# Optimization experiments

Measured on AMD Instinct MI355X. Metric: run time of the kernel, lower is better.

## Reference

```python
import jax, jax.numpy as jnp
import numpy as np
from jax import lax

D = 1024
T = 1024
B = 8


def setup_inputs() -> dict:
    key = jax.random.key(0)
    ks = jax.random.split(key, 4)
    x = jax.random.normal(ks[0], (T, B, D), dtype=jnp.float32)
    h0 = jnp.zeros((B, D), dtype=jnp.float32)
    # xavier-ish scale for input projections, small orthogonal-like scale for W_h
    xav = float(np.sqrt(2.0 / (D + D)))
    W_alpha = jax.random.normal(ks[1], (D, D), dtype=jnp.float32) * xav
    b_alpha = jnp.full((D,), 2.0, dtype=jnp.float32)  # init_alpha_bias=2.0
    W_h = jax.random.normal(ks[2], (D, D), dtype=jnp.float32) * (0.5 / np.sqrt(D))
    W_x = jax.random.normal(ks[3], (D, D), dtype=jnp.float32) * xav
    b = jnp.zeros((D,), dtype=jnp.float32)
    return {"x": x, "h0": h0, "W_alpha": W_alpha, "b_alpha": b_alpha,
            "W_h": W_h, "W_x": W_x, "b": b}


def reference(x, h0, W_alpha, b_alpha, W_h, W_x, b):
    # x: [T,B,D], h0: [B,D]; E63a nonlinear delta recurrence.
    # Precompute input-dependent parts (parallel over T), scan the recurrence.
    alpha_all = jax.nn.sigmoid(jnp.einsum('tbd,ed->tbe', x, W_alpha) + b_alpha)  # [T,B,D]
    wx_all = jnp.einsum('tbd,ed->tbe', x, W_x) + b                               # [T,B,D]

    def step(h_prev, inp):
        alpha, wx = inp
        v = jnp.tanh(h_prev @ W_h.T + wx)          # nonlinear value in h
        h_new = alpha * h_prev + (1.0 - alpha) * v  # complementary gate
        out = h_new * jax.nn.silu(h_new)            # gated output
        return h_new, (h_new, out)

    _, (hs, outs) = lax.scan(step, h0, (alpha_all, wx_all))
    h = jnp.concatenate([h0[None], hs], axis=0)  # [T+1,B,D] (matches torch path)
    return outs, h
```

## Files before the change

### kernel.cpp

```cpp
#include <hip/hip_runtime.h>
#include <hip/hip_bf16.h>
#include <hip/hip_cooperative_groups.h>

typedef __attribute__((ext_vector_type(8))) short bf16x8;
typedef __attribute__((ext_vector_type(4))) float f32x4;
typedef __attribute__((ext_vector_type(4))) unsigned int u32x4;

#define D_ 1024
#define T_ 1024
#define B_ 8
#define M_ (T_ * B_)

__device__ __forceinline__ float ldv(const float* p) { return *p; }
__device__ __forceinline__ float ldv(const __hip_bfloat16* p) { return __bfloat162float(*p); }
__device__ __forceinline__ void stv(float* p, float v) { *p = v; }
__device__ __forceinline__ void stv(__hip_bfloat16* p, float v) { *p = __float2bfloat16(v); }

__device__ __forceinline__ u32x4 ld_chunk(const unsigned* p) {
  u32x4 v;
  asm volatile("global_load_dwordx4 %0, %1, off sc0 sc1" : "=v"(v) : "v"(p) : "memory");
  return v;
}
__device__ __forceinline__ void st_word(unsigned* p, unsigned v) {
  asm volatile("global_store_dword %0, %1, off sc0 sc1" :: "v"(p), "v"(v) : "memory");
}
__device__ __forceinline__ void wait_vm0() {
  asm volatile("s_waitcnt vmcnt(0)" ::: "memory");
}
__device__ __forceinline__ void bar_lds() {
  asm volatile("s_waitcnt lgkmcnt(0)\n\ts_barrier" ::: "memory");
  __builtin_amdgcn_sched_barrier(0);
}

__global__ __launch_bounds__(256) void conv_bf16(const float* __restrict__ in,
                                                 __hip_bfloat16* __restrict__ out,
                                                 int n8)
{
  int i = blockIdx.x * blockDim.x + threadIdx.x;
  const int stride = gridDim.x * blockDim.x;
  for (; i < n8; i += stride) {
    const f32x4* p = reinterpret_cast<const f32x4*>(in + (size_t)i * 8);
    f32x4 a = p[0], b = p[1];
    union { bf16x8 v; __hip_bfloat16 e[8]; } u;
#pragma unroll
    for (int j = 0; j < 4; ++j) {
      u.e[j] = __float2bfloat16(a[j]);
      u.e[j + 4] = __float2bfloat16(b[j]);
    }
    *reinterpret_cast<bf16x8*>(out + (size_t)i * 8) = u.v;
  }
}

template <typename ST>
__global__ __launch_bounds__(256) void gemm_front(
    const __hip_bfloat16* __restrict__ xb,
    const __hip_bfloat16* __restrict__ Wab,
    const float* __restrict__ ba,
    const __hip_bfloat16* __restrict__ Wxb,
    const float* __restrict__ bbias,
    ST* __restrict__ alpha_out,
    ST* __restrict__ wx_out)
{
  const int tid = threadIdx.x;
  const int lane = tid & 63;
  const int w = tid >> 6;
  const int r = lane & 15;
  const int g = lane >> 4;
  const bool isA = blockIdx.y < 8;
  const int m0 = blockIdx.x * 128 + (w >> 1) * 64;
  const int n0 = (blockIdx.y & 7) * 128 + (w & 1) * 64;
  const __hip_bfloat16* __restrict__ W = isA ? Wab : Wxb;
  ST* __restrict__ outp = isA ? alpha_out : wx_out;

  f32x4 acc[4][4] = {};

  const __hip_bfloat16* aBase = xb + (size_t)(m0 + r) * D_ + g * 8;
  const __hip_bfloat16* bBase = W + (size_t)(n0 + r) * D_ + g * 8;

  for (int k = 0; k < D_; k += 32) {
    bf16x8 a[4], b[4];
#pragma unroll
    for (int mt = 0; mt < 4; ++mt)
      a[mt] = *reinterpret_cast<const bf16x8*>(aBase + (size_t)mt * 16 * D_ + k);
#pragma unroll
    for (int nt = 0; nt < 4; ++nt)
      b[nt] = *reinterpret_cast<const bf16x8*>(bBase + (size_t)nt * 16 * D_ + k);
#pragma unroll
    for (int mt = 0; mt < 4; ++mt)
#pragma unroll
      for (int nt = 0; nt < 4; ++nt)
        acc[mt][nt] = __builtin_amdgcn_mfma_f32_16x16x32_bf16(a[mt], b[nt], acc[mt][nt], 0, 0, 0);
  }

#pragma unroll
  for (int nt = 0; nt < 4; ++nt) {
    const int col = n0 + nt * 16 + r;
    const float bias = isA ? ba[col] : bbias[col];
#pragma unroll
    for (int mt = 0; mt < 4; ++mt) {
      const int row = m0 + mt * 16 + g * 4;
#pragma unroll
      for (int i = 0; i < 4; ++i) {
        float v = acc[mt][nt][i] + bias;
        if (isA) v = 1.0f / (1.0f + expf(-v));
        stv(outp + (size_t)(row + i) * D_ + col, v);
      }
    }
  }
}

template <typename ST>
__global__ __launch_bounds__(256) void scan_rec(
    const float* __restrict__ h0,
    const float* __restrict__ Wh,
    const ST* __restrict__ alpha_all,
    const ST* __restrict__ wx_all,
    unsigned* __restrict__ ring,
    float* __restrict__ out_outs,
    float* __restrict__ out_h)
{
  __shared__ __align__(16) unsigned short W_lds[64 * 1024];
  __shared__ __align__(16) unsigned short h_lds[1024];
  __shared__ float C_lds[4][64];

  const int tid = threadIdx.x;
  const int lane = tid & 63;
  const int w = tid >> 6;
  const int r = lane & 15;
  const int g = lane >> 4;
  const int bb = blockIdx.x & 7;
  const int s = blockIdx.x >> 3;
  const int e0 = s * 64;

  for (int idx = tid; idx < 64 * 128; idx += 256) {
    const int row = idx >> 7;
    const int k8 = (idx & 127) * 8;
    const f32x4* p = reinterpret_cast<const f32x4*>(Wh + (size_t)(e0 + row) * D_ + k8);
    f32x4 a = p[0], bv = p[1];
    union { bf16x8 v; __hip_bfloat16 e[8]; } u;
#pragma unroll
    for (int j = 0; j < 4; ++j) {
      u.e[j] = __float2bfloat16(a[j]);
      u.e[j + 4] = __float2bfloat16(bv[j]);
    }
    const unsigned byteoff = ((unsigned)row * 2048u + (unsigned)k8 * 2u) ^ (((unsigned)row & 7u) << 4);
    *reinterpret_cast<bf16x8*>(reinterpret_cast<char*>(W_lds) + byteoff) = u.v;
  }

  float h_f = 0.0f, wx_c = 0.0f, al_c = 0.0f;
  if (tid < 64) {
    const int e = e0 + tid;
    h_f = h0[bb * D_ + e];
    out_h[(size_t)bb * D_ + e] = h_f;
    const unsigned short hb = ((__hip_bfloat16_raw)__float2bfloat16(h_f)).x;
    h_lds[e] = hb;
    st_word(ring + (size_t)bb * 1024 + e, (unsigned)hb | (1u << 16));
    wx_c = ldv(wx_all + (size_t)bb * D_ + e);
    al_c = ldv(alpha_all + (size_t)bb * D_ + e);
  }
  __syncthreads();

  for (int t = 0; t < T_; ++t) {
    const unsigned want = (unsigned)(t + 1);
    const int kk = w * 256 + lane * 8;
    if (lane < 32 && (kk >> 6) != s) {
      const unsigned* cp = ring + ((size_t)(t & 1) * B_ + bb) * 1024 + kk;
      u32x4 A, Bv;
      int bail = 0;
      for (;;) {
        A = ld_chunk(cp);
        Bv = ld_chunk(cp + 4);
        wait_vm0();
        const bool ok = (A[0] >> 16) == want && (A[1] >> 16) == want &&
                        (A[2] >> 16) == want && (A[3] >> 16) == want &&
                        (Bv[0] >> 16) == want && (Bv[1] >> 16) == want &&
                        (Bv[2] >> 16) == want && (Bv[3] >> 16) == want;
        if (__all(ok)) break;
        if (++bail > (1 << 20)) break;
      }
      u32x4 hw;
      hw[0] = (A[0] & 0xffffu) | (A[1] << 16);
      hw[1] = (A[2] & 0xffffu) | (A[3] << 16);
      hw[2] = (Bv[0] & 0xffffu) | (Bv[1] << 16);
      hw[3] = (Bv[2] & 0xffffu) | (Bv[3] << 16);
      *reinterpret_cast<u32x4*>(&h_lds[kk]) = hw;
    }
    asm volatile("s_waitcnt lgkmcnt(0)" ::: "memory");
    __builtin_amdgcn_sched_barrier(0);

    f32x4 acc[4] = {};
#pragma unroll
    for (int kt = 0; kt < 8; ++kt) {
      const int k = w * 256 + kt * 32 + g * 8;
      bf16x8 afrag = {};
      if (r == 0)
        afrag = *reinterpret_cast<const bf16x8*>(&h_lds[k]);
#pragma unroll
      for (int nt = 0; nt < 4; ++nt) {
        const unsigned row = (unsigned)(nt * 16 + r);
        const unsigned byteoff = (row * 2048u + (unsigned)k * 2u) ^ ((row & 7u) << 4);
        bf16x8 bfrag = *reinterpret_cast<const bf16x8*>(
            reinterpret_cast<const char*>(W_lds) + byteoff);
        acc[nt] = __builtin_amdgcn_mfma_f32_16x16x32_bf16(afrag, bfrag, acc[nt], 0, 0, 0);
      }
    }
    if (g == 0) {
#pragma unroll
      for (int nt = 0; nt < 4; ++nt)
        C_lds[w][nt * 16 + r] = acc[nt][0];
    }
    bar_lds();

    if (tid < 64) {
      const int e = e0 + tid;
      const float y = C_lds[0][tid] + C_lds[1][tid] + C_lds[2][tid] + C_lds[3][tid];
      const float v = tanhf(y + wx_c);
      h_f = al_c * h_f + (1.0f - al_c) * v;
      const unsigned short hb = ((__hip_bfloat16_raw)__float2bfloat16(h_f)).x;
      h_lds[e] = hb;
      st_word(ring + ((size_t)((t + 1) & 1) * B_ + bb) * 1024 + e,
              (unsigned)hb | ((unsigned)(t + 2) << 16));
      const float sg = 1.0f / (1.0f + expf(-h_f));
      const float o = h_f * h_f * sg;
      out_h[(size_t)(t + 1) * (B_ * D_) + (size_t)bb * D_ + e] = h_f;
      out_outs[(size_t)t * (B_ * D_) + (size_t)bb * D_ + e] = o;
      if (t + 1 < T_) {
        wx_c = ldv(wx_all + (size_t)((t + 1) * B_ + bb) * D_ + e);
        al_c = ldv(alpha_all + (size_t)((t + 1) * B_ + bb) * D_ + e);
      }
    }
    bar_lds();
  }
}

template <typename ST>
static void launch_all(const float* x, const float* h0, const float* Wa,
                       const float* ba, const float* Wh, const float* Wx,
                       const float* bb, __hip_bfloat16* xb, __hip_bfloat16* Wab,
                       __hip_bfloat16* Wxb, ST* alpha_buf, ST* wx_buf,
                       unsigned* ring, float* out_outs, float* out_h,
                       hipStream_t stream)
{
  const size_t ringBytes = (size_t)2 * B_ * 1024 * 4;
  hipMemsetAsync(ring, 0, ringBytes, stream);
  conv_bf16<<<dim3(2048), dim3(256), 0, stream>>>(x, xb, M_ * D_ / 8);
  conv_bf16<<<dim3(512), dim3(256), 0, stream>>>(Wa, Wab, D_ * D_ / 8);
  conv_bf16<<<dim3(512), dim3(256), 0, stream>>>(Wx, Wxb, D_ * D_ / 8);
  gemm_front<ST><<<dim3(64, 16), dim3(256), 0, stream>>>(xb, Wab, ba, Wxb, bb,
                                                         alpha_buf, wx_buf);
  void* args[] = {(void*)&h0,     (void*)&Wh,   (void*)&alpha_buf,
                  (void*)&wx_buf, (void*)&ring, (void*)&out_outs,
                  (void*)&out_h};
  hipLaunchCooperativeKernel(reinterpret_cast<void*>(&scan_rec<ST>), dim3(128),
                             dim3(256), args, 0, stream);
}

extern "C" void kernel_launch(void* const* d_in, const int* in_sizes, int n_in,
                              void* d_out, int out_size, void* d_ws,
                              size_t ws_size, hipStream_t stream)
{
  const float* x = (const float*)d_in[0];
  const float* h0 = (const float*)d_in[1];
  const float* Wa = (const float*)d_in[2];
  const float* ba = (const float*)d_in[3];
  const float* Wh = (const float*)d_in[4];
  const float* Wx = (const float*)d_in[5];
  const float* bb = (const float*)d_in[6];

  float* out_outs = (float*)d_out;
  float* out_h = out_outs + (size_t)T_ * B_ * D_;

  char* ws = (char*)d_ws;
  const size_t nMD = (size_t)M_ * D_;
  const size_t nDD = (size_t)D_ * D_;

  __hip_bfloat16* xb = (__hip_bfloat16*)ws;
  __hip_bfloat16* Wab = (__hip_bfloat16*)(ws + nMD * 2);
  __hip_bfloat16* Wxb = (__hip_bfloat16*)(ws + nMD * 2 + nDD * 2);
  char* rest = ws + nMD * 2 + 2 * nDD * 2;

  const size_t ringBytes = (size_t)2 * B_ * 1024 * 4;
  const size_t needF32 = (size_t)(rest - ws) + 2 * nMD * 4 + ringBytes;

  if (ws_size >= needF32) {
    float* alpha_buf = (float*)rest;
    float* wx_buf = (float*)(rest + nMD * 4);
    unsigned* ring = (unsigned*)(rest + 2 * nMD * 4);
    launch_all<float>(x, h0, Wa, ba, Wh, Wx, bb, xb, Wab, Wxb, alpha_buf,
                      wx_buf, ring, out_outs, out_h, stream);
  } else {
    __hip_bfloat16* alpha_buf = (__hip_bfloat16*)rest;
    __hip_bfloat16* wx_buf = (__hip_bfloat16*)(rest + nMD * 2);
    unsigned* ring = (unsigned*)(rest + 2 * nMD * 2);
    launch_all<__hip_bfloat16>(x, h0, Wa, ba, Wh, Wx, bb, xb, Wab, Wxb,
                               alpha_buf, wx_buf, ring, out_outs, out_h,
                               stream);
  }
}
```

Before: 1.911 ms.

## Split recurrence matvec by output rows per wave, double-buffer h, use fast tanh/sigmoid

```diff
diff --git a/kernel.cpp b/kernel.cpp
--- a/kernel.cpp
+++ b/kernel.cpp
@@ -30,6 +30,16 @@
 __device__ __forceinline__ void bar_lds() {
   asm volatile("s_waitcnt lgkmcnt(0)\n\ts_barrier" ::: "memory");
   __builtin_amdgcn_sched_barrier(0);
+}
+__device__ __forceinline__ float exp2_fast(float x) {
+  float r;
+  asm("v_exp_f32 %0, %1" : "=v"(r) : "v"(x));
+  return r;
+}
+__device__ __forceinline__ float rcp_fast(float x) {
+  float r;
+  asm("v_rcp_f32 %0, %1" : "=v"(r) : "v"(x));
+  return r;
 }
 
 __global__ __launch_bounds__(256) void conv_bf16(const float* __restrict__ in,
@@ -120,8 +130,7 @@
     float* __restrict__ out_h)
 {
   __shared__ __align__(16) unsigned short W_lds[64 * 1024];
-  __shared__ __align__(16) unsigned short h_lds[1024];
-  __shared__ float C_lds[4][64];
+  __shared__ __align__(16) unsigned short h_lds[2][1024];
 
   const int tid = threadIdx.x;
   const int lane = tid & 63;
@@ -147,16 +156,18 @@
     *reinterpret_cast<bf16x8*>(reinterpret_cast<char*>(W_lds) + byteoff) = u.v;
   }
 
-  float h_f = 0.0f, wx_c = 0.0f, al_c = 0.0f;
-  if (tid < 64) {
-    const int e = e0 + tid;
+  const int e = e0 + w * 16 + r;
+  float h_f = 0.0f, wx_c = 0.0f, p_c = 0.0f, q_c = 0.0f;
+  if (g == 0) {
     h_f = h0[bb * D_ + e];
     out_h[(size_t)bb * D_ + e] = h_f;
     const unsigned short hb = ((__hip_bfloat16_raw)__float2bfloat16(h_f)).x;
-    h_lds[e] = hb;
+    h_lds[0][e] = hb;
     st_word(ring + (size_t)bb * 1024 + e, (unsigned)hb | (1u << 16));
     wx_c = ldv(wx_all + (size_t)bb * D_ + e);
-    al_c = ldv(alpha_all + (size_t)bb * D_ + e);
+    const float al = ldv(alpha_all + (size_t)bb * D_ + e);
+    p_c = al * h_f;
+    q_c = 1.0f - al;
   }
   __syncthreads();
 
@@ -183,53 +194,45 @@
       hw[1] = (A[2] & 0xffffu) | (A[3] << 16);
       hw[2] = (Bv[0] & 0xffffu) | (Bv[1] << 16);
       hw[3] = (Bv[2] & 0xffffu) | (Bv[3] << 16);
-      *reinterpret_cast<u32x4*>(&h_lds[kk]) = hw;
-    }
-    asm volatile("s_waitcnt lgkmcnt(0)" ::: "memory");
-    __builtin_amdgcn_sched_barrier(0);
+      *reinterpret_cast<u32x4*>(&h_lds[t & 1][kk]) = hw;
+    }
+    bar_lds();
 
     f32x4 acc[4] = {};
 #pragma unroll
-    for (int kt = 0; kt < 8; ++kt) {
-      const int k = w * 256 + kt * 32 + g * 8;
+    for (int kt = 0; kt < 32; ++kt) {
+      const int k = kt * 32 + g * 8;
       bf16x8 afrag = {};
       if (r == 0)
-        afrag = *reinterpret_cast<const bf16x8*>(&h_lds[k]);
-#pragma unroll
-      for (int nt = 0; nt < 4; ++nt) {
-        const unsigned row = (unsigned)(nt * 16 + r);
-        const unsigned byteoff = (row * 2048u + (unsigned)k * 2u) ^ ((row & 7u) << 4);
-        bf16x8 bfrag = *reinterpret_cast<const bf16x8*>(
-            reinterpret_cast<const char*>(W_lds) + byteoff);
-        acc[nt] = __builtin_amdgcn_mfma_f32_16x16x32_bf16(afrag, bfrag, acc[nt], 0, 0, 0);
-      }
-    }
+        afrag = *reinterpret_cast<const bf16x8*>(&h_lds[t & 1][k]);
+      const unsigned row = (unsigned)(w * 16 + r);
+      const unsigned byteoff = (row * 2048u + (unsigned)k * 2u) ^ ((r & 7u) << 4);
+      bf16x8 bfrag = *reinterpret_cast<const bf16x8*>(
+          reinterpret_cast<const char*>(W_lds) + byteoff);
+      acc[kt & 3] = __builtin_amdgcn_mfma_f32_16x16x32_bf16(afrag, bfrag, acc[kt & 3], 0, 0, 0);
+    }
+
     if (g == 0) {
-#pragma unroll
-      for (int nt = 0; nt < 4; ++nt)
-        C_lds[w][nt * 16 + r] = acc[nt][0];
-    }
-    bar_lds();
-
-    if (tid < 64) {
-      const int e = e0 + tid;
-      const float y = C_lds[0][tid] + C_lds[1][tid] + C_lds[2][tid] + C_lds[3][tid];
-      const float v = tanhf(y + wx_c);
-      h_f = al_c * h_f + (1.0f - al_c) * v;
+      const float y = acc[0][0] + acc[1][0] + acc[2][0] + acc[3][0];
+      const float xs = (y + wx_c) * 2.8853900817779268f;
+      const float ex = exp2_fast(xs);
+      const float tv = fmaf(-2.0f, rcp_fast(ex + 1.0f), 1.0f);
+      h_f = fmaf(q_c, tv, p_c);
       const unsigned short hb = ((__hip_bfloat16_raw)__float2bfloat16(h_f)).x;
-      h_lds[e] = hb;
       st_word(ring + ((size_t)((t + 1) & 1) * B_ + bb) * 1024 + e,
               (unsigned)hb | ((unsigned)(t + 2) << 16));
-      const float sg = 1.0f / (1.0f + expf(-h_f));
+      h_lds[(t + 1) & 1][e] = hb;
+      const float sg = rcp_fast(1.0f + exp2_fast(h_f * -1.4426950408889634f));
       const float o = h_f * h_f * sg;
       out_h[(size_t)(t + 1) * (B_ * D_) + (size_t)bb * D_ + e] = h_f;
       out_outs[(size_t)t * (B_ * D_) + (size_t)bb * D_ + e] = o;
       if (t + 1 < T_) {
         wx_c = ldv(wx_all + (size_t)((t + 1) * B_ + bb) * D_ + e);
-        al_c = ldv(alpha_all + (size_t)((t + 1) * B_ + bb) * D_ + e);
+        const float al = ldv(alpha_all + (size_t)((t + 1) * B_ + bb) * D_ + e);
+        p_c = al * h_f;
+        q_c = 1.0f - al;
       }
     }
-    bar_lds();
   }
 }
 
```

After: 2.444 ms. 1.28x slower.
